# Performance work log

Hardware: AMD Instinct MI355X
Metric: run time of the kernel (lower is better)

## Reference

```python
import jax, jax.numpy as jnp
import numpy as np

B, T, C, H = 4, 2048, 1024, 16
D = C // H  # head dim = 64


def _layernorm(x, g, b, eps=1e-5):
    mu = jnp.mean(x, axis=-1, keepdims=True)
    var = jnp.var(x, axis=-1, keepdims=True)
    return (x - mu) * jax.lax.rsqrt(var + eps) * g + b


def setup_inputs() -> dict:
    key = jax.random.key(0)
    ks = jax.random.split(key, 8)
    s = 0.02
    return {
        "x": jax.random.normal(ks[0], (B, T, C), dtype=jnp.float32),
        "ln1_g": jnp.ones((C,), jnp.float32),
        "ln1_b": jnp.zeros((C,), jnp.float32),
        "W_qkv": jax.random.normal(ks[1], (C, 3 * C), dtype=jnp.float32) * s,
        "b_qkv": jnp.zeros((3 * C,), jnp.float32),
        "W_o": jax.random.normal(ks[2], (C, C), dtype=jnp.float32) * s,
        "b_o": jnp.zeros((C,), jnp.float32),
        "ln2_g": jnp.ones((C,), jnp.float32),
        "ln2_b": jnp.zeros((C,), jnp.float32),
        "W_fc": jax.random.normal(ks[3], (C, 4 * C), dtype=jnp.float32) * s,
        "b_fc": jnp.zeros((4 * C,), jnp.float32),
        "W_pr": jax.random.normal(ks[4], (4 * C, C), dtype=jnp.float32) * s,
        "b_pr": jnp.zeros((C,), jnp.float32),
    }


def reference(x, ln1_g, ln1_b, W_qkv, b_qkv, W_o, b_o, ln2_g, ln2_b, W_fc, b_fc, W_pr, b_pr):
    # --- attention sub-block ---
    h = _layernorm(x, ln1_g, ln1_b)
    qkv = h @ W_qkv + b_qkv                       # [B,T,3C]
    q, k, v = jnp.split(qkv, 3, axis=-1)
    q = q.reshape(B, T, H, D).transpose(0, 2, 1, 3)  # [B,H,T,D]
    k = k.reshape(B, T, H, D).transpose(0, 2, 1, 3)
    v = v.reshape(B, T, H, D).transpose(0, 2, 1, 3)
    att = jnp.einsum("bhqd,bhkd->bhqk", q, k) * (1.0 / jnp.sqrt(jnp.float32(D)))
    causal = jnp.tril(jnp.ones((T, T), dtype=bool))
    att = jnp.where(causal, att, jnp.float32(-jnp.inf))
    att = jax.nn.softmax(att, axis=-1)
    y = jnp.einsum("bhqk,bhkd->bhqd", att, v)     # [B,H,T,D]
    y = y.transpose(0, 2, 1, 3).reshape(B, T, C)
    y = y @ W_o + b_o
    x = x + y
    # --- FFN sub-block ---
    h2 = _layernorm(x, ln2_g, ln2_b)
    f = jax.nn.gelu(h2 @ W_fc + b_fc, approximate=False)  # nn.GELU default = exact
    f = f @ W_pr + b_pr
    return x + f
```

## Files before the change

kernel.cpp:

```cpp
#include <hip/hip_runtime.h>
#include <math.h>

#define Bz 4
#define Tz 2048
#define Cz 1024
#define Hz 16
#define Dz 64
#define MTOK (Bz*Tz)

typedef __attribute__((ext_vector_type(8))) short short8;
typedef __attribute__((ext_vector_type(4))) short short4v;
typedef __attribute__((ext_vector_type(4))) float f32x4;

typedef unsigned int u32_g __attribute__((address_space(1)));
typedef unsigned int u32_l __attribute__((address_space(3)));

__device__ __forceinline__ unsigned short f2bf(float f) {
    unsigned int u = __float_as_uint(f);
    u += 0x7fffu + ((u >> 16) & 1u);
    return (unsigned short)(u >> 16);
}
__device__ __forceinline__ float bf2f(unsigned short h) {
    return __uint_as_float((unsigned int)h << 16);
}

__device__ __forceinline__ void async_cp16(const unsigned short* g, unsigned short* l) {
    __builtin_amdgcn_global_load_lds((const u32_g*)g, (u32_l*)l, 16, 0, 0);
}

#define BARX() __builtin_amdgcn_s_barrier()
#define VMCM(n) asm volatile("s_waitcnt vmcnt(" #n ")" ::: "memory")

__global__ void transpose_w(const float* __restrict__ W, unsigned short* __restrict__ Wt,
                            int K, int N) {
    __shared__ float tile[32][33];
    int n0 = blockIdx.x * 32, k0 = blockIdx.y * 32;
    int tx = threadIdx.x, ty = threadIdx.y;
    #pragma unroll
    for (int i = 0; i < 4; i++)
        tile[ty + i * 8][tx] = W[(size_t)(k0 + ty + i * 8) * N + n0 + tx];
    __syncthreads();
    #pragma unroll
    for (int i = 0; i < 4; i++)
        Wt[(size_t)(n0 + ty + i * 8) * K + k0 + tx] = f2bf(tile[tx][ty + i * 8]);
}

__global__ void transpose_v(const unsigned short* __restrict__ in, unsigned short* __restrict__ out) {
    __shared__ unsigned short tile[64][68];
    const int bh = blockIdx.x;
    const int t0 = blockIdx.y * 64;
    const int tid = threadIdx.x;
    const int r4 = tid >> 4;
    const int c4 = tid & 15;
    #pragma unroll
    for (int p = 0; p < 4; p++) {
        const int r = p * 16 + r4;
        *(short4v*)&tile[r][c4 * 4] =
            *(const short4v*)&in[((size_t)bh * Tz + t0 + r) * Dz + c4 * 4];
    }
    __syncthreads();
    #pragma unroll
    for (int p = 0; p < 4; p++) {
        const int d = p * 16 + r4;
        short4v o;
        #pragma unroll
        for (int j = 0; j < 4; j++) o[j] = tile[c4 * 4 + j][d];
        *(short4v*)&out[((size_t)bh * Dz + d) * Tz + t0 + c4 * 4] = o;
    }
}

__global__ void ln_kernel(const float* __restrict__ x, const float* __restrict__ g,
                          const float* __restrict__ bb, unsigned short* __restrict__ out) {
    int tok = blockIdx.x, tid = threadIdx.x;
    const float4 v = ((const float4*)(x + (size_t)tok * Cz))[tid];
    float s = v.x + v.y + v.z + v.w;
    float sq = v.x * v.x + v.y * v.y + v.z * v.z + v.w * v.w;
    #pragma unroll
    for (int m = 1; m < 64; m <<= 1) { s += __shfl_xor(s, m); sq += __shfl_xor(sq, m); }
    __shared__ float red[8];
    int lane = tid & 63, wid = tid >> 6;
    if (!lane) { red[wid] = s; red[4 + wid] = sq; }
    __syncthreads();
    s = red[0] + red[1] + red[2] + red[3];
    sq = red[4] + red[5] + red[6] + red[7];
    float mu = s * (1.0f / Cz);
    float var = sq * (1.0f / Cz) - mu * mu;
    float rs = rsqrtf(var + 1e-5f);
    float4 gv = ((const float4*)g)[tid];
    float4 bv = ((const float4*)bb)[tid];
    short4v o;
    o[0] = f2bf((v.x - mu) * rs * gv.x + bv.x);
    o[1] = f2bf((v.y - mu) * rs * gv.y + bv.y);
    o[2] = f2bf((v.z - mu) * rs * gv.z + bv.z);
    o[3] = f2bf((v.w - mu) * rs * gv.w + bv.w);
    *(short4v*)(out + (size_t)tok * Cz + tid * 4) = o;
}

#define MODE_QKV 0
#define MODE_RESID 1
#define MODE_GELU 2

template <int MODE>
__launch_bounds__(512, 1)
__global__ void gemm_p(const unsigned short* __restrict__ A, const unsigned short* __restrict__ Bt,
                       int lda, int K, int N, const float* __restrict__ bias,
                       float* __restrict__ outf, unsigned short* __restrict__ outb,
                       const float* __restrict__ resid,
                       unsigned short* __restrict__ qo, unsigned short* __restrict__ ko,
                       unsigned short* __restrict__ vo) {
    __shared__ __align__(16) unsigned short LDS[4 * 12288];
    const int tid = threadIdx.x;
    const int lane = tid & 63;
    const int wid = tid >> 6;
    const int quad = lane >> 4, l15 = lane & 15;
    const int gm = wid >> 1, gn = wid & 1;
    const int id = blockIdx.x;
    const int rr = id >> 3;
    const int m0 = ((id & 7) * 4 + (rr & 3)) * 256;
    const int n0 = (rr >> 2) * 128;
    const int NT = K >> 5;

    const int lseg = (tid & 3) ^ ((tid >> 3) & 3);
    const int srow = tid >> 2;
    const unsigned short* Ag0 = A + (size_t)(m0 + srow) * lda + lseg * 8;
    const unsigned short* Ag1 = A + (size_t)(m0 + 128 + srow) * lda + lseg * 8;
    const unsigned short* Bg0 = Bt + (size_t)(n0 + srow) * lda + lseg * 8;

    int offA[4], offB[4];
    #pragma unroll
    for (int mi = 0; mi < 4; mi++) {
        const int ra = gm * 64 + mi * 16 + l15;
        offA[mi] = ra * 32 + ((quad ^ ((ra >> 1) & 3)) << 3);
    }
    #pragma unroll
    for (int ni = 0; ni < 4; ni++) {
        const int rb = gn * 64 + ni * 16 + l15;
        offB[ni] = 8192 + rb * 32 + ((quad ^ ((rb >> 1) & 3)) << 3);
    }

    f32x4 acc[4][4] = {};
    short8 afA[4], bfA[4], afB[4], bfB[4];

#define STG(tt) do { \
    unsigned short* sp_ = LDS + (((unsigned)(tt)) & 3u) * 12288; \
    const size_t kof_ = (size_t)(tt) * 32; \
    async_cp16(Ag0 + kof_, sp_ + tid * 8); \
    async_cp16(Ag1 + kof_, sp_ + 4096 + tid * 8); \
    async_cp16(Bg0 + kof_, sp_ + 8192 + tid * 8); } while (0)
#define RDS(afX, bfX, tt) do { \
    const unsigned short* sp_ = LDS + (((unsigned)(tt)) & 3u) * 12288; \
    _Pragma("unroll") for (int mi = 0; mi < 4; mi++) afX[mi] = *(const short8*)(sp_ + offA[mi]); \
    _Pragma("unroll") for (int ni = 0; ni < 4; ni++) bfX[ni] = *(const short8*)(sp_ + offB[ni]); } while (0)
#define MMS(afX, bfX) do { \
    __builtin_amdgcn_s_setprio(1); \
    _Pragma("unroll") for (int mi = 0; mi < 4; mi++) \
        _Pragma("unroll") for (int ni = 0; ni < 4; ni++) \
            acc[mi][ni] = __builtin_amdgcn_mfma_f32_16x16x32_bf16(afX[mi], bfX[ni], acc[mi][ni], 0, 0, 0); \
    __builtin_amdgcn_s_setprio(0); } while (0)

    STG(0); STG(1); STG(2);
    VMCM(6);
    BARX();
    RDS(afA, bfA, 0);

    for (int t = 0; t < NT; t += 2) {
        if (t + 2 < NT) { VMCM(3); } else { VMCM(0); }
        BARX();
        if (t + 3 < NT) STG(t + 3);
        RDS(afB, bfB, t + 1);
        MMS(afA, bfA);
        if (t + 2 < NT) { VMCM(3); }
        BARX();
        if (t + 4 < NT) STG(t + 4);
        if (t + 2 < NT) RDS(afA, bfA, t + 2);
        MMS(afB, bfB);
    }
#undef STG
#undef RDS
#undef MMS

    float bv[4];
    #pragma unroll
    for (int ni = 0; ni < 4; ni++) bv[ni] = bias[n0 + gn * 64 + ni * 16 + l15];

    if constexpr (MODE == MODE_QKV) {
        const int colb = n0 + gn * 64;
        const int which = colb >> 10;
        const int hh = (colb & 1023) >> 6;
        unsigned short* dst = (which == 0) ? qo : (which == 1) ? ko : vo;
        #pragma unroll
        for (int mi = 0; mi < 4; mi++) {
            #pragma unroll
            for (int r = 0; r < 4; r++) {
                const int row = m0 + gm * 64 + mi * 16 + quad * 4 + r;
                const int b_ = row >> 11, tt = row & 2047;
                unsigned short* rp = dst + ((size_t)(b_ * Hz + hh) * Tz + tt) * Dz;
                #pragma unroll
                for (int ni = 0; ni < 4; ni++)
                    rp[ni * 16 + l15] = f2bf(acc[mi][ni][r] + bv[ni]);
            }
        }
    } else if constexpr (MODE == MODE_RESID) {
        #pragma unroll
        for (int mi = 0; mi < 4; mi++) {
            #pragma unroll
            for (int r = 0; r < 4; r++) {
                const int row = m0 + gm * 64 + mi * 16 + quad * 4 + r;
                float* rp = outf + (size_t)row * N + n0 + gn * 64;
                const float* rr_ = resid + (size_t)row * N + n0 + gn * 64;
                #pragma unroll
                for (int ni = 0; ni < 4; ni++) {
                    const int c = ni * 16 + l15;
                    rp[c] = acc[mi][ni][r] + bv[ni] + rr_[c];
                }
            }
        }
    } else {
        #pragma unroll
        for (int mi = 0; mi < 4; mi++) {
            #pragma unroll
            for (int r = 0; r < 4; r++) {
                const int row = m0 + gm * 64 + mi * 16 + quad * 4 + r;
                unsigned short* rp = outb + (size_t)row * N + n0 + gn * 64;
                #pragma unroll
                for (int ni = 0; ni < 4; ni++) {
                    float val = acc[mi][ni][r] + bv[ni];
                    float c = val * (1.0f + 0.044715f * val * val);
                    float e = __expf(1.5957691216057308f * c);
                    rp[ni * 16 + l15] = f2bf(val * e / (1.0f + e));
                }
            }
        }
    }
}

#define ATT_SC 0.18033688011112042f
__launch_bounds__(256)
__global__ void attn_kernel(const unsigned short* __restrict__ qb, const unsigned short* __restrict__ kb,
                            const unsigned short* __restrict__ vt, unsigned short* __restrict__ y) {
    __shared__ __align__(16) unsigned short Klds[64 * 64];
    __shared__ __align__(16) unsigned short Vtl[64 * 64];
    __shared__ __align__(16) unsigned short Plds[4][16 * 72];
    const int tid = threadIdx.x;
    const int lane = tid & 63, wid = tid >> 6;
    const int quad = lane >> 4, l15 = lane & 15;
    const int bh = blockIdx.x & 63;
    const int qt = 15 - (int)(blockIdx.x >> 6);
    const size_t baseT = (size_t)bh * Tz;
    const size_t vbase = (size_t)bh * Dz;
    const int qb0 = qt * 128;

    short8 qf[2][2];
    {
        const unsigned short* q0p = qb + (baseT + qb0 + wid * 16 + l15) * Dz + quad * 8;
        qf[0][0] = *(const short8*)q0p;
        qf[0][1] = *(const short8*)(q0p + 32);
        const unsigned short* q1p = q0p + (size_t)64 * Dz;
        qf[1][0] = *(const short8*)q1p;
        qf[1][1] = *(const short8*)(q1p + 32);
    }

    f32x4 o[2][4] = {};
    float lsum[2][4] = {{0.f,0.f,0.f,0.f},{0.f,0.f,0.f,0.f}};

    const int srow = lane >> 3;
    const int swz = ((lane & 7) ^ srow) * 8;
    const unsigned short* kg0 = kb + (baseT + wid * 8 + srow) * Dz + swz;
    const unsigned short* kg1 = kg0 + (size_t)32 * Dz;
    const unsigned short* vg0 = vt + (vbase + wid * 8 + srow) * Tz + swz;
    const unsigned short* vg1 = vg0 + (size_t)32 * Tz;
    unsigned short* kl0 = &Klds[wid * 512 + lane * 8];
    unsigned short* kl1 = kl0 + 2048;
    unsigned short* vl0 = &Vtl[wid * 512 + lane * 8];
    unsigned short* vl1 = vl0 + 2048;

    const int nchunk = 2 * qt + 2;

    for (int ci = 0; ci < nchunk; ci++) {
        const int k0 = ci * 64;
        async_cp16(kg0 + (size_t)k0 * Dz, kl0);
        async_cp16(kg1 + (size_t)k0 * Dz, kl1);
        async_cp16(vg0 + k0, vl0);
        async_cp16(vg1 + k0, vl1);
        __syncthreads();

        #pragma unroll
        for (int t = 0; t < 2; t++) {
            if (t == 0 && ci == nchunk - 1) continue;
            const bool diag = (ci == nchunk - 2 + t);

            f32x4 s[4];
            #pragma unroll
            for (int c = 0; c < 4; c++) {
                const int rk = c * 16 + l15;
                short8 kf0 = *(const short8*)&Klds[rk * 64 + ((quad ^ (rk & 7)) * 8)];
                short8 kf1 = *(const short8*)&Klds[rk * 64 + (((quad + 4) ^ (rk & 7)) * 8)];
                f32x4 z = {};
                z = __builtin_amdgcn_mfma_f32_16x16x32_bf16(qf[t][0], kf0, z, 0, 0, 0);
                s[c] = __builtin_amdgcn_mfma_f32_16x16x32_bf16(qf[t][1], kf1, z, 0, 0, 0);
            }
            const int qr = qb0 + t * 64 + wid * 16 + quad * 4;
            #pragma unroll
            for (int c = 0; c < 4; c++)
                #pragma unroll
                for (int r = 0; r < 4; r++) {
                    float p = exp2f(s[c][r] * ATT_SC);
                    if (diag) {
                        int key = k0 + c * 16 + l15;
                        p = (key <= qr + r) ? p : 0.f;
                    }
                    s[c][r] = p;
                    lsum[t][r] += p;
                }
            unsigned short* P = Plds[wid];
            #pragma unroll
            for (int c = 0; c < 4; c++)
                #pragma unroll
                for (int r = 0; r < 4; r++)
                    P[(quad * 4 + r) * 72 + c * 16 + l15] = f2bf(s[c][r]);
            short8 pf0 = *(const short8*)&P[l15 * 72 + quad * 8];
            short8 pf1 = *(const short8*)&P[l15 * 72 + 32 + quad * 8];
            #pragma unroll
            for (int nc = 0; nc < 4; nc++) {
                const int rv = nc * 16 + l15;
                short8 vf0 = *(const short8*)&Vtl[rv * 64 + ((quad ^ (rv & 7)) * 8)];
                short8 vf1 = *(const short8*)&Vtl[rv * 64 + (((quad + 4) ^ (rv & 7)) * 8)];
                o[t][nc] = __builtin_amdgcn_mfma_f32_16x16x32_bf16(pf0, vf0, o[t][nc], 0, 0, 0);
                o[t][nc] = __builtin_amdgcn_mfma_f32_16x16x32_bf16(pf1, vf1, o[t][nc], 0, 0, 0);
            }
        }
        __syncthreads();
    }

    const int b_ = bh >> 4, hh = bh & 15;
    #pragma unroll
    for (int t = 0; t < 2; t++)
        #pragma unroll
        for (int r = 0; r < 4; r++) {
            float ls = lsum[t][r];
            #pragma unroll
            for (int m = 1; m < 16; m <<= 1) ls += __shfl_xor(ls, m);
            float inv = 1.0f / ls;
            size_t tok = (size_t)qb0 + t * 64 + wid * 16 + quad * 4 + r;
            unsigned short* yr = y + ((size_t)b_ * Tz + tok) * Cz + hh * Dz;
            #pragma unroll
            for (int nc = 0; nc < 4; nc++)
                yr[nc * 16 + l15] = f2bf(o[t][nc][r] * inv);
        }
}

extern "C" void kernel_launch(void* const* d_in, const int* in_sizes, int n_in,
                              void* d_out, int out_size, void* d_ws, size_t ws_size,
                              hipStream_t stream) {
    const float* x    = (const float*)d_in[0];
    const float* ln1g = (const float*)d_in[1];
    const float* ln1b = (const float*)d_in[2];
    const float* Wqkv = (const float*)d_in[3];
    const float* bqkv = (const float*)d_in[4];
    const float* Wo   = (const float*)d_in[5];
    const float* bo   = (const float*)d_in[6];
    const float* ln2g = (const float*)d_in[7];
    const float* ln2b = (const float*)d_in[8];
    const float* Wfc  = (const float*)d_in[9];
    const float* bfc  = (const float*)d_in[10];
    const float* Wpr  = (const float*)d_in[11];
    const float* bpr  = (const float*)d_in[12];
    float* out = (float*)d_out;

    char* ws = (char*)d_ws;
    size_t off = 0;
    auto alloc = [&](size_t bytes) { void* p = ws + off; off += (bytes + 255) & ~(size_t)255; return p; };
    unsigned short* wqkv_t = (unsigned short*)alloc((size_t)3072 * 1024 * 2);
    unsigned short* wo_t   = (unsigned short*)alloc((size_t)1024 * 1024 * 2);
    unsigned short* wfc_t  = (unsigned short*)alloc((size_t)4096 * 1024 * 2);
    unsigned short* wpr_t  = (unsigned short*)alloc((size_t)1024 * 4096 * 2);
    unsigned short* h1     = (unsigned short*)alloc((size_t)MTOK * Cz * 2);
    unsigned short* qbuf   = (unsigned short*)alloc((size_t)MTOK * Cz * 2);
    unsigned short* kbuf   = (unsigned short*)alloc((size_t)MTOK * Cz * 2);
    unsigned short* vbuf   = (unsigned short*)alloc((size_t)MTOK * Cz * 2);
    unsigned short* ybuf   = (unsigned short*)alloc((size_t)MTOK * Cz * 2);
    float*          x1     = (float*)alloc((size_t)MTOK * Cz * 4);
    unsigned short* h2     = (unsigned short*)alloc((size_t)MTOK * Cz * 2);
    unsigned short* fbuf   = (unsigned short*)alloc((size_t)MTOK * 4096 * 2);
    unsigned short* vtmp   = fbuf;

    dim3 tb(32, 8);
    transpose_w<<<dim3(3072 / 32, 1024 / 32), tb, 0, stream>>>(Wqkv, wqkv_t, 1024, 3072);
    transpose_w<<<dim3(1024 / 32, 1024 / 32), tb, 0, stream>>>(Wo, wo_t, 1024, 1024);
    transpose_w<<<dim3(4096 / 32, 1024 / 32), tb, 0, stream>>>(Wfc, wfc_t, 1024, 4096);
    transpose_w<<<dim3(1024 / 32, 4096 / 32), tb, 0, stream>>>(Wpr, wpr_t, 4096, 1024);

    ln_kernel<<<MTOK, 256, 0, stream>>>(x, ln1g, ln1b, h1);
    gemm_p<MODE_QKV><<<768, 512, 0, stream>>>(h1, wqkv_t, 1024, 1024, 3072, bqkv,
                                              nullptr, nullptr, nullptr, qbuf, kbuf, vtmp);
    transpose_v<<<dim3(64, 32), 256, 0, stream>>>(vtmp, vbuf);
    attn_kernel<<<1024, 256, 0, stream>>>(qbuf, kbuf, vbuf, ybuf);
    gemm_p<MODE_RESID><<<256, 512, 0, stream>>>(ybuf, wo_t, 1024, 1024, 1024, bo,
                                                x1, nullptr, x, nullptr, nullptr, nullptr);
    ln_kernel<<<MTOK, 256, 0, stream>>>(x1, ln2g, ln2b, h2);
    gemm_p<MODE_GELU><<<1024, 512, 0, stream>>>(h2, wfc_t, 1024, 1024, 4096, bfc,
                                                nullptr, fbuf, nullptr, nullptr, nullptr, nullptr);
    gemm_p<MODE_RESID><<<256, 512, 0, stream>>>(fbuf, wpr_t, 4096, 4096, 1024, bpr,
                                                out, nullptr, x1, nullptr, nullptr, nullptr);
}
```

Baseline: 517.8 us.

## Load B operand directly from global in MFMA fragment layout, bypassing LDS

Weights are now pre-packed into an MFMA-fragment-ordered bf16 layout, so each wave loads its B fragments straight from global memory into registers instead of staging them through LDS. The GEMM warp grid changes from 4x2 to 2x4 with a 256-wide N tile, and the FC GEMM uses a larger 256x256 block tile. This cuts LDS traffic and LDS footprint for B but relies on L2 for reuse of B across blocks and adds register pressure, and the wait counts have to track the mixed global and LDS loads correctly.

Measured after the change: 516.1 us. Within noise of the previous version (-0.3%).

```diff
diff --git a/kernel.cpp b/kernel.cpp
--- a/kernel.cpp
+++ b/kernel.cpp
@@ -1,5 +1,6 @@
 #include <hip/hip_runtime.h>
 #include <math.h>
+#include <stdint.h>
 
 #define Bz 4
 #define Tz 2048
@@ -28,21 +29,23 @@
     __builtin_amdgcn_global_load_lds((const u32_g*)g, (u32_l*)l, 16, 0, 0);
 }
 
-#define BARX() __builtin_amdgcn_s_barrier()
+#define BARX() asm volatile("s_barrier" ::: "memory")
 #define VMCM(n) asm volatile("s_waitcnt vmcnt(" #n ")" ::: "memory")
 
-__global__ void transpose_w(const float* __restrict__ W, unsigned short* __restrict__ Wt,
-                            int K, int N) {
-    __shared__ float tile[32][33];
-    int n0 = blockIdx.x * 32, k0 = blockIdx.y * 32;
-    int tx = threadIdx.x, ty = threadIdx.y;
-    #pragma unroll
-    for (int i = 0; i < 4; i++)
-        tile[ty + i * 8][tx] = W[(size_t)(k0 + ty + i * 8) * N + n0 + tx];
-    __syncthreads();
-    #pragma unroll
-    for (int i = 0; i < 4; i++)
-        Wt[(size_t)(n0 + ty + i * 8) * K + k0 + tx] = f2bf(tile[tx][ty + i * 8]);
+__global__ void transpose_wf(const float* __restrict__ W, unsigned short* __restrict__ Bf,
+                             int K, int N) {
+    const int nf = blockIdx.x;
+    const int k0 = blockIdx.y * 128;
+    const int tid = threadIdx.x;
+    const int ktl = tid >> 6, lane = tid & 63;
+    const int col = nf * 16 + (lane & 15);
+    const int kk = k0 + ktl * 32 + (lane >> 4) * 8;
+    const int KT = K >> 5;
+    short8 o;
+    #pragma unroll
+    for (int j = 0; j < 8; j++)
+        o[j] = (short)f2bf(W[(size_t)(kk + j) * N + col]);
+    *(short8*)&Bf[(((size_t)nf * KT + (k0 >> 5) + ktl) * 64 + lane) * 8] = o;
 }
 
 __global__ void transpose_v(const unsigned short* __restrict__ in, unsigned short* __restrict__ out) {
@@ -100,84 +103,98 @@
 #define MODE_RESID 1
 #define MODE_GELU 2
 
-template <int MODE>
+template <int MODE, int WM>
 __launch_bounds__(512, 1)
-__global__ void gemm_p(const unsigned short* __restrict__ A, const unsigned short* __restrict__ Bt,
-                       int lda, int K, int N, const float* __restrict__ bias,
-                       float* __restrict__ outf, unsigned short* __restrict__ outb,
-                       const float* __restrict__ resid,
-                       unsigned short* __restrict__ qo, unsigned short* __restrict__ ko,
-                       unsigned short* __restrict__ vo) {
-    __shared__ __align__(16) unsigned short LDS[4 * 12288];
+__global__ void gemm_bg(const unsigned short* __restrict__ A, const unsigned short* __restrict__ Bf,
+                        int K, int N, const float* __restrict__ bias,
+                        float* __restrict__ outf, unsigned short* __restrict__ outb,
+                        const float* __restrict__ resid,
+                        unsigned short* __restrict__ qo, unsigned short* __restrict__ ko,
+                        unsigned short* __restrict__ vo) {
+    constexpr int MI = WM / 16;
+    constexpr int BM = 2 * WM;
+    constexpr int SLOT = BM * 32;
+    constexpr int AC = BM / 128;
+    constexpr int MT = 8192 / BM;
+    constexpr int MT8 = MT / 8;
+    __shared__ __align__(16) unsigned short LDS[4 * SLOT];
+
     const int tid = threadIdx.x;
     const int lane = tid & 63;
     const int wid = tid >> 6;
     const int quad = lane >> 4, l15 = lane & 15;
-    const int gm = wid >> 1, gn = wid & 1;
+    const int gm = wid >> 2, gn = wid & 3;
     const int id = blockIdx.x;
     const int rr = id >> 3;
-    const int m0 = ((id & 7) * 4 + (rr & 3)) * 256;
-    const int n0 = (rr >> 2) * 128;
+    const int m0 = ((id & 7) * MT8 + (rr % MT8)) * BM;
+    const int n0 = (rr / MT8) * 256;
     const int NT = K >> 5;
+    const int KT = K >> 5;
 
     const int lseg = (tid & 3) ^ ((tid >> 3) & 3);
     const int srow = tid >> 2;
-    const unsigned short* Ag0 = A + (size_t)(m0 + srow) * lda + lseg * 8;
-    const unsigned short* Ag1 = A + (size_t)(m0 + 128 + srow) * lda + lseg * 8;
-    const unsigned short* Bg0 = Bt + (size_t)(n0 + srow) * lda + lseg * 8;
-
-    int offA[4], offB[4];
-    #pragma unroll
-    for (int mi = 0; mi < 4; mi++) {
-        const int ra = gm * 64 + mi * 16 + l15;
+    const unsigned short* Ag0 = A + (size_t)(m0 + srow) * K + lseg * 8;
+    const unsigned short* Ag1 = A + (size_t)(m0 + 128 + srow) * K + lseg * 8;
+
+    int offA[MI];
+    #pragma unroll
+    for (int mi = 0; mi < MI; mi++) {
+        const int ra = gm * WM + mi * 16 + l15;
         offA[mi] = ra * 32 + ((quad ^ ((ra >> 1) & 3)) << 3);
     }
-    #pragma unroll
-    for (int ni = 0; ni < 4; ni++) {
-        const int rb = gn * 64 + ni * 16 + l15;
-        offB[ni] = 8192 + rb * 32 + ((quad ^ ((rb >> 1) & 3)) << 3);
-    }
-
-    f32x4 acc[4][4] = {};
-    short8 afA[4], bfA[4], afB[4], bfB[4];
-
-#define STG(tt) do { \
-    unsigned short* sp_ = LDS + (((unsigned)(tt)) & 3u) * 12288; \
+
+    const int nfg = (n0 >> 4) + gn * 4;
+    const unsigned short* Bp[4];
+    #pragma unroll
+    for (int ni = 0; ni < 4; ni++)
+        Bp[ni] = Bf + ((size_t)(nfg + ni) * KT) * 512 + lane * 8;
+
+    f32x4 acc[MI][4] = {};
+    short8 af[MI], bfP[4], bfQ[4];
+
+#define GLB(bfX) do { _Pragma("unroll") for (int ni = 0; ni < 4; ni++) { \
+    asm volatile("global_load_dwordx4 %0, %1, off" \
+        : "=&v"(bfX[ni]) : "v"((unsigned long long)(uintptr_t)Bp[ni]) : "memory"); \
+    Bp[ni] += 512; } } while (0)
+#define STG(tt) do { unsigned short* sp_ = LDS + (((unsigned)(tt)) & 3u) * SLOT; \
     const size_t kof_ = (size_t)(tt) * 32; \
     async_cp16(Ag0 + kof_, sp_ + tid * 8); \
-    async_cp16(Ag1 + kof_, sp_ + 4096 + tid * 8); \
-    async_cp16(Bg0 + kof_, sp_ + 8192 + tid * 8); } while (0)
-#define RDS(afX, bfX, tt) do { \
-    const unsigned short* sp_ = LDS + (((unsigned)(tt)) & 3u) * 12288; \
-    _Pragma("unroll") for (int mi = 0; mi < 4; mi++) afX[mi] = *(const short8*)(sp_ + offA[mi]); \
-    _Pragma("unroll") for (int ni = 0; ni < 4; ni++) bfX[ni] = *(const short8*)(sp_ + offB[ni]); } while (0)
-#define MMS(afX, bfX) do { \
+    if constexpr (AC == 2) async_cp16(Ag1 + kof_, sp_ + 4096 + tid * 8); } while (0)
+#define RDS(tt) do { const unsigned short* sp_ = LDS + (((unsigned)(tt)) & 3u) * SLOT; \
+    _Pragma("unroll") for (int mi = 0; mi < MI; mi++) af[mi] = *(const short8*)(sp_ + offA[mi]); } while (0)
+#define MMS(bfX) do { \
     __builtin_amdgcn_s_setprio(1); \
-    _Pragma("unroll") for (int mi = 0; mi < 4; mi++) \
+    _Pragma("unroll") for (int mi = 0; mi < MI; mi++) \
         _Pragma("unroll") for (int ni = 0; ni < 4; ni++) \
-            acc[mi][ni] = __builtin_amdgcn_mfma_f32_16x16x32_bf16(afX[mi], bfX[ni], acc[mi][ni], 0, 0, 0); \
+            acc[mi][ni] = __builtin_amdgcn_mfma_f32_16x16x32_bf16(af[mi], bfX[ni], acc[mi][ni], 0, 0, 0); \
     __builtin_amdgcn_s_setprio(0); } while (0)
-
+#define WAITV(tt) do { \
+    if ((tt) == 0)            { if constexpr (AC == 2) VMCM(4); else VMCM(2); } \
+    else if ((tt) >= NT - 2)  { VMCM(0); } \
+    else                      { if constexpr (AC == 2) VMCM(2); else VMCM(1); } } while (0)
+
+    GLB(bfP);
     STG(0); STG(1); STG(2);
-    VMCM(6);
-    BARX();
-    RDS(afA, bfA, 0);
 
     for (int t = 0; t < NT; t += 2) {
-        if (t + 2 < NT) { VMCM(3); } else { VMCM(0); }
+        WAITV(t);
         BARX();
+        if (t + 1 < NT) GLB(bfQ);
         if (t + 3 < NT) STG(t + 3);
-        RDS(afB, bfB, t + 1);
-        MMS(afA, bfA);
-        if (t + 2 < NT) { VMCM(3); }
+        RDS(t);
+        MMS(bfP);
+        WAITV(t + 1);
         BARX();
+        if (t + 2 < NT) GLB(bfP);
         if (t + 4 < NT) STG(t + 4);
-        if (t + 2 < NT) RDS(afA, bfA, t + 2);
-        MMS(afB, bfB);
-    }
+        RDS(t + 1);
+        MMS(bfQ);
+    }
+#undef GLB
 #undef STG
 #undef RDS
 #undef MMS
+#undef WAITV
 
     float bv[4];
     #pragma unroll
@@ -189,10 +206,10 @@
         const int hh = (colb & 1023) >> 6;
         unsigned short* dst = (which == 0) ? qo : (which == 1) ? ko : vo;
         #pragma unroll
-        for (int mi = 0; mi < 4; mi++) {
+        for (int mi = 0; mi < MI; mi++) {
             #pragma unroll
             for (int r = 0; r < 4; r++) {
-                const int row = m0 + gm * 64 + mi * 16 + quad * 4 + r;
+                const int row = m0 + gm * WM + mi * 16 + quad * 4 + r;
                 const int b_ = row >> 11, tt = row & 2047;
                 unsigned short* rp = dst + ((size_t)(b_ * Hz + hh) * Tz + tt) * Dz;
                 #pragma unroll
@@ -202,10 +219,10 @@
         }
     } else if constexpr (MODE == MODE_RESID) {
         #pragma unroll
-        for (int mi = 0; mi < 4; mi++) {
+        for (int mi = 0; mi < MI; mi++) {
             #pragma unroll
             for (int r = 0; r < 4; r++) {
-                const int row = m0 + gm * 64 + mi * 16 + quad * 4 + r;
+                const int row = m0 + gm * WM + mi * 16 + quad * 4 + r;
                 float* rp = outf + (size_t)row * N + n0 + gn * 64;
                 const float* rr_ = resid + (size_t)row * N + n0 + gn * 64;
                 #pragma unroll
@@ -217,10 +234,10 @@
         }
     } else {
         #pragma unroll
-        for (int mi = 0; mi < 4; mi++) {
+        for (int mi = 0; mi < MI; mi++) {
             #pragma unroll
             for (int r = 0; r < 4; r++) {
-                const int row = m0 + gm * 64 + mi * 16 + quad * 4 + r;
+                const int row = m0 + gm * WM + mi * 16 + quad * 4 + r;
                 unsigned short* rp = outb + (size_t)row * N + n0 + gn * 64;
                 #pragma unroll
                 for (int ni = 0; ni < 4; ni++) {
@@ -384,22 +401,21 @@
     unsigned short* fbuf   = (unsigned short*)alloc((size_t)MTOK * 4096 * 2);
     unsigned short* vtmp   = fbuf;
 
-    dim3 tb(32, 8);
-    transpose_w<<<dim3(3072 / 32, 1024 / 32), tb, 0, stream>>>(Wqkv, wqkv_t, 1024, 3072);
-    transpose_w<<<dim3(1024 / 32, 1024 / 32), tb, 0, stream>>>(Wo, wo_t, 1024, 1024);
-    transpose_w<<<dim3(4096 / 32, 1024 / 32), tb, 0, stream>>>(Wfc, wfc_t, 1024, 4096);
-    transpose_w<<<dim3(1024 / 32, 4096 / 32), tb, 0, stream>>>(Wpr, wpr_t, 4096, 1024);
+    transpose_wf<<<dim3(3072 / 16, 1024 / 128), 256, 0, stream>>>(Wqkv, wqkv_t, 1024, 3072);
+    transpose_wf<<<dim3(1024 / 16, 1024 / 128), 256, 0, stream>>>(Wo, wo_t, 1024, 1024);
+    transpose_wf<<<dim3(4096 / 16, 1024 / 128), 256, 0, stream>>>(Wfc, wfc_t, 1024, 4096);
+    transpose_wf<<<dim3(1024 / 16, 4096 / 128), 256, 0, stream>>>(Wpr, wpr_t, 4096, 1024);
 
     ln_kernel<<<MTOK, 256, 0, stream>>>(x, ln1g, ln1b, h1);
-    gemm_p<MODE_QKV><<<768, 512, 0, stream>>>(h1, wqkv_t, 1024, 1024, 3072, bqkv,
-                                              nullptr, nullptr, nullptr, qbuf, kbuf, vtmp);
+    gemm_bg<MODE_QKV, 64><<<768, 512, 0, stream>>>(h1, wqkv_t, 1024, 3072, bqkv,
+                                                   nullptr, nullptr, nullptr, qbuf, kbuf, vtmp);
     transpose_v<<<dim3(64, 32), 256, 0, stream>>>(vtmp, vbuf);
     attn_kernel<<<1024, 256, 0, stream>>>(qbuf, kbuf, vbuf, ybuf);
-    gemm_p<MODE_RESID><<<256, 512, 0, stream>>>(ybuf, wo_t, 1024, 1024, 1024, bo,
-                                                x1, nullptr, x, nullptr, nullptr, nullptr);
+    gemm_bg<MODE_RESID, 64><<<256, 512, 0, stream>>>(ybuf, wo_t, 1024, 1024, bo,
+                                                     x1, nullptr, x, nullptr, nullptr, nullptr);
     ln_kernel<<<MTOK, 256, 0, stream>>>(x1, ln2g, ln2b, h2);
-    gemm_p<MODE_GELU><<<1024, 512, 0, stream>>>(h2, wfc_t, 1024, 1024, 4096, bfc,
-                                                nullptr, fbuf, nullptr, nullptr, nullptr, nullptr);
-    gemm_p<MODE_RESID><<<256, 512, 0, stream>>>(fbuf, wpr_t, 4096, 4096, 1024, bpr,
-                                                out, nullptr, x1, nullptr, nullptr, nullptr);
-}
+    gemm_bg<MODE_GELU, 128><<<512, 512, 0, stream>>>(h2, wfc_t, 1024, 4096, bfc,
+                                                     nullptr, fbuf, nullptr, nullptr, nullptr, nullptr);
+    gemm_bg<MODE_RESID, 64><<<256, 512, 0, stream>>>(fbuf, wpr_t, 4096, 1024, bpr,
+                                                     out, nullptr, x1, nullptr, nullptr, nullptr);
+}
```
